# Kernel optimization log

Hardware: AMD Instinct MI355X
Metric: run time of the kernel (lower is better)

## Reference

```python
import jax, jax.numpy as jnp
import numpy as np

B, S, HIDDEN = 2, 2048, 2048
N_HEADS, N_KV_HEADS = 32, 8
HEAD_DIM = HIDDEN // N_HEADS          # 64
HALF = HEAD_DIM // 2                  # 32
N_REP = N_HEADS // N_KV_HEADS         # 4
NEG_INF = -1e9


def setup_inputs() -> dict:
    key = jax.random.key(0)
    ks = jax.random.split(key, 5)
    scale = 0.02
    x = jax.random.normal(ks[0], (B, S, HIDDEN), dtype=jnp.float32)
    wq = jax.random.normal(ks[1], (HIDDEN, N_HEADS * HEAD_DIM), dtype=jnp.float32) * scale
    wk = jax.random.normal(ks[2], (HIDDEN, N_KV_HEADS * HEAD_DIM), dtype=jnp.float32) * scale
    wv = jax.random.normal(ks[3], (HIDDEN, N_KV_HEADS * HEAD_DIM), dtype=jnp.float32) * scale
    wo = jax.random.normal(ks[4], (HIDDEN, HIDDEN), dtype=jnp.float32) * scale
    # Llama rotary frequencies: theta = 10000^{-2i/d}, angles = pos * theta
    inv_freq = 1.0 / (10000.0 ** (np.arange(0, HEAD_DIM, 2, dtype=np.float32) / HEAD_DIM))
    angles = np.arange(S, dtype=np.float32)[:, None] * inv_freq[None, :]  # [S, HALF]
    freqs_cos = jnp.asarray(np.cos(angles), dtype=jnp.float32)
    freqs_sin = jnp.asarray(np.sin(angles), dtype=jnp.float32)
    mask = jnp.tril(jnp.ones((S, S), dtype=bool))[None, None]  # causal [1,1,S,S]
    return {"x": x, "wq": wq, "wk": wk, "wv": wv, "wo": wo,
            "freqs_cos": freqs_cos, "freqs_sin": freqs_sin, "mask": mask}


def _apply_rope(t, cos, sin):
    # t: [B, S, H, HEAD_DIM]; cos/sin: [S, HALF] -> broadcast [1, S, 1, HALF]
    tr, ti = t[..., ::2], t[..., 1::2]           # real/imag halves (interleaved pairing)
    c = cos[None, :, None, :]
    s = sin[None, :, None, :]
    out_r = tr * c - ti * s
    out_i = tr * s + ti * c
    out = jnp.stack([out_r, out_i], axis=-1)     # [B,S,H,HALF,2]
    return out.reshape(t.shape)                  # re-interleave


def reference(x, wq, wk, wv, wo, freqs_cos, freqs_sin, mask):
    b, s, _ = x.shape
    xq = (x @ wq).reshape(b, s, N_HEADS, HEAD_DIM)
    xk = (x @ wk).reshape(b, s, N_KV_HEADS, HEAD_DIM)
    xv = (x @ wv).reshape(b, s, N_KV_HEADS, HEAD_DIM)
    xq = _apply_rope(xq, freqs_cos, freqs_sin)
    xk = _apply_rope(xk, freqs_cos, freqs_sin)
    # repeat_kv: interleave-repeat kv heads to match query heads
    xk = jnp.repeat(xk, N_REP, axis=2)           # [B,S,N_HEADS,HEAD_DIM]
    xv = jnp.repeat(xv, N_REP, axis=2)
    q = jnp.transpose(xq, (0, 2, 1, 3))          # [B,H,S,D]
    k = jnp.transpose(xk, (0, 2, 1, 3))
    v = jnp.transpose(xv, (0, 2, 1, 3))
    attn = jnp.einsum('bhqd,bhkd->bhqk', q, k) / jnp.sqrt(jnp.float32(HEAD_DIM))
    attn = attn + (1.0 - mask.astype(attn.dtype)) * NEG_INF  # keras Softmax masking
    attn = jax.nn.softmax(attn, axis=-1)
    out = jnp.einsum('bhqk,bhkd->bhqd', attn, v)
    out = jnp.transpose(out, (0, 2, 1, 3)).reshape(b, s, HIDDEN)
    return out @ wo
```

## Files before the change

kernel.cpp:

```cpp
#include <hip/hip_runtime.h>
#include <cstdint>
#include <cstddef>

#define S_LEN 2048
#define HIDDEN 2048
#define NH 32
#define NKV 8
#define HD 64
#define QKV_W 3072

typedef __bf16 bf16;
typedef __bf16 bf16x8 __attribute__((ext_vector_type(8)));
typedef __bf16 bf16x4 __attribute__((ext_vector_type(4)));
typedef float f32x4 __attribute__((ext_vector_type(4)));

__device__ __forceinline__ void async16(const bf16* g, bf16* l) {
  __builtin_amdgcn_global_load_lds((const __attribute__((address_space(1))) void*)g,
                                   (__attribute__((address_space(3))) void*)l, 16, 0, 0);
}

__device__ __forceinline__ int swz8(int row, int col) {
  return (((col >> 3) ^ (row & 7)) << 3) | (col & 7);
}

__global__ void cast_x_kernel(const float* __restrict__ in, bf16* __restrict__ out, int n4) {
  int i = blockIdx.x * blockDim.x + threadIdx.x;
  if (i >= n4) return;
  f32x4 v = ((const f32x4*)in)[i];
  bf16x4 o;
  o[0] = (bf16)v[0]; o[1] = (bf16)v[1]; o[2] = (bf16)v[2]; o[3] = (bf16)v[3];
  ((bf16x4*)out)[i] = o;
}

__global__ void transpose_cast_kernel(const float* __restrict__ in, bf16* __restrict__ out,
                                      int K, int N) {
  __shared__ float tile[32][33];
  const int n0 = blockIdx.x * 32, k0 = blockIdx.y * 32;
  const int tx = threadIdx.x, ty = threadIdx.y;
#pragma unroll
  for (int i = 0; i < 32; i += 8)
    tile[ty + i][tx] = in[(size_t)(k0 + ty + i) * N + n0 + tx];
  __syncthreads();
#pragma unroll
  for (int i = 0; i < 32; i += 8)
    out[(size_t)(n0 + ty + i) * K + k0 + tx] = (bf16)tile[tx][ty + i];
}

__global__ void vt_kernel(const bf16* __restrict__ qkv, bf16* __restrict__ vt) {
  __shared__ bf16 tile[32][33];
  const int s0 = blockIdx.x * 32, c0 = blockIdx.y * 32, b = blockIdx.z;
  const int tx = threadIdx.x, ty = threadIdx.y;
#pragma unroll
  for (int i = 0; i < 32; i += 8)
    tile[ty + i][tx] = qkv[((size_t)b * S_LEN + s0 + ty + i) * QKV_W + 2560 + c0 + tx];
  __syncthreads();
#pragma unroll
  for (int i = 0; i < 32; i += 8)
    vt[((size_t)b * 512 + c0 + ty + i) * S_LEN + s0 + tx] = tile[tx][ty + i];
}

template <int OUT_BF16>
__global__ __launch_bounds__(256) void gemm_bt_kernel(const bf16* __restrict__ A,
                                                      const bf16* __restrict__ Bt,
                                                      void* __restrict__ Cv,
                                                      int M, int N, int K) {
  __shared__ bf16 Al[128 * 32];
  __shared__ bf16 Bl[128 * 32];
  const int tid = threadIdx.x;
  const int lane = tid & 63, w = tid >> 6;
  const int quad = lane >> 4, l16 = lane & 15;
  const int m0 = blockIdx.y * 128, n0 = blockIdx.x * 128;
  const int wm = (w >> 1) * 64, wn = (w & 1) * 64;
  f32x4 acc[4][4] = {};
  const int srow = tid >> 2, scol = (tid & 3) * 8;
  const bf16* Ar0 = A + (size_t)(m0 + srow) * K + scol;
  const bf16* Ar1 = A + (size_t)(m0 + 64 + srow) * K + scol;
  const bf16* Br0 = Bt + (size_t)(n0 + srow) * K + scol;
  const bf16* Br1 = Bt + (size_t)(n0 + 64 + srow) * K + scol;
  bf16* al0 = Al + tid * 8;
  bf16* al1 = Al + 2048 + tid * 8;
  bf16* bl0 = Bl + tid * 8;
  bf16* bl1 = Bl + 2048 + tid * 8;
  for (int kt = 0; kt < K; kt += 32) {
    __syncthreads();
    async16(Ar0 + kt, al0);
    async16(Ar1 + kt, al1);
    async16(Br0 + kt, bl0);
    async16(Br1 + kt, bl1);
    __syncthreads();
    bf16x8 a[4], b[4];
#pragma unroll
    for (int mi = 0; mi < 4; ++mi)
      a[mi] = *(const bf16x8*)(Al + (wm + mi * 16 + l16) * 32 + quad * 8);
#pragma unroll
    for (int ni = 0; ni < 4; ++ni)
      b[ni] = *(const bf16x8*)(Bl + (wn + ni * 16 + l16) * 32 + quad * 8);
#pragma unroll
    for (int mi = 0; mi < 4; ++mi)
#pragma unroll
      for (int ni = 0; ni < 4; ++ni)
        acc[mi][ni] = __builtin_amdgcn_mfma_f32_16x16x32_bf16(a[mi], b[ni], acc[mi][ni], 0, 0, 0);
  }
#pragma unroll
  for (int mi = 0; mi < 4; ++mi)
#pragma unroll
    for (int ni = 0; ni < 4; ++ni)
#pragma unroll
      for (int i = 0; i < 4; ++i) {
        const int row = m0 + wm + mi * 16 + quad * 4 + i;
        const int col = n0 + wn + ni * 16 + l16;
        if (OUT_BF16)
          ((bf16*)Cv)[(size_t)row * N + col] = (bf16)acc[mi][ni][i];
        else
          ((float*)Cv)[(size_t)row * N + col] = acc[mi][ni][i];
      }
}

__global__ void rope_kernel(bf16* __restrict__ qkv, const float* __restrict__ cosp,
                            const float* __restrict__ sinp, int total) {
  int idx = blockIdx.x * blockDim.x + threadIdx.x;
  if (idx >= total) return;
  const int row = idx / 320;
  const int col = (idx - row * 320) * 8;
  const int s = row & (S_LEN - 1);
  const int j0 = (col >> 1) & 31;
  bf16* ptr = qkv + (size_t)row * QKV_W + col;
  bf16x8 v = *(bf16x8*)ptr;
#pragma unroll
  for (int u = 0; u < 4; ++u) {
    const float tr = (float)v[2 * u], ti = (float)v[2 * u + 1];
    const float c = cosp[s * 32 + j0 + u], sn = sinp[s * 32 + j0 + u];
    v[2 * u] = (bf16)(tr * c - ti * sn);
    v[2 * u + 1] = (bf16)(tr * sn + ti * c);
  }
  *(bf16x8*)ptr = v;
}

__global__ __launch_bounds__(256) void attn_kernel(const bf16* __restrict__ qkv,
                                                   const bf16* __restrict__ vt,
                                                   bf16* __restrict__ out) {
  __shared__ bf16 Kl[64 * 64];
  __shared__ bf16 Vl[64 * 64];
  __shared__ bf16 Pl[4][32 * 64];
  const int tid = threadIdx.x;
  const int lane = tid & 63, w = tid >> 6;
  const int quad = lane >> 4, l16 = lane & 15;
  int id = blockIdx.x;
  const int kvh = id & 7; id >>= 3;
  const int gx = id & 7; id >>= 3;
  const int rep = id & 3; const int b = id >> 2;
  const int h = kvh * 4 + rep;
  const bf16* Qbase = qkv + ((size_t)b * S_LEN) * QKV_W + h * HD;
  const bf16* Kbase = qkv + ((size_t)b * S_LEN) * QKV_W + 2048 + kvh * HD;
  const bf16* Vtb = vt + ((size_t)b * 512 + kvh * 64) * S_LEN;
  const int srow = tid >> 3;
  const int gcol = ((tid & 7) ^ (srow & 7)) * 8;
  const bf16* Ksrc0 = Kbase + (size_t)srow * QKV_W + gcol;
  const bf16* Ksrc1 = Kbase + (size_t)(srow + 32) * QKV_W + gcol;
  const bf16* Vsrc0 = Vtb + (size_t)srow * S_LEN + gcol;
  const bf16* Vsrc1 = Vtb + (size_t)(srow + 32) * S_LEN + gcol;

  for (int pass = 0; pass < 2; ++pass) {
    const int qt = pass ? (15 - gx) : gx;
    const int qbase = qt * 128 + w * 32;
    bf16x8 aq[2][2];
#pragma unroll
    for (int g = 0; g < 2; ++g) {
      const size_t qr = (size_t)(qbase + g * 16 + l16) * QKV_W;
      aq[g][0] = *(const bf16x8*)(Qbase + qr + quad * 8);
      aq[g][1] = *(const bf16x8*)(Qbase + qr + 32 + quad * 8);
    }
    float lsum0 = 0.f, lsum1 = 0.f;
    f32x4 o[2][4] = {};

    const int nt = 2 * qt + 2;
    for (int t = 0; t < nt; ++t) {
      const int kt = t * 64;
      __syncthreads();
      async16(Ksrc0 + (size_t)kt * QKV_W, Kl + tid * 8);
      async16(Ksrc1 + (size_t)kt * QKV_W, Kl + 2048 + tid * 8);
      async16(Vsrc0 + kt, Vl + tid * 8);
      async16(Vsrc1 + kt, Vl + 2048 + tid * 8);
      __syncthreads();
      const bool on0 = kt <= qbase + 15;
      const bool on1 = kt <= qbase + 31;
      if (!on1) continue;
      f32x4 c[2][4] = {};
#pragma unroll
      for (int j = 0; j < 4; ++j) {
        const int kr = j * 16 + l16;
        const bf16x8 bk0 = *(const bf16x8*)&Kl[kr * 64 + swz8(kr, quad * 8)];
        const bf16x8 bk1 = *(const bf16x8*)&Kl[kr * 64 + swz8(kr, 32 + quad * 8)];
        c[1][j] = __builtin_amdgcn_mfma_f32_16x16x32_bf16(bk0, aq[1][0], c[1][j], 0, 0, 0);
        c[1][j] = __builtin_amdgcn_mfma_f32_16x16x32_bf16(bk1, aq[1][1], c[1][j], 0, 0, 0);
        if (on0) {
          c[0][j] = __builtin_amdgcn_mfma_f32_16x16x32_bf16(bk0, aq[0][0], c[0][j], 0, 0, 0);
          c[0][j] = __builtin_amdgcn_mfma_f32_16x16x32_bf16(bk1, aq[0][1], c[0][j], 0, 0, 0);
        }
      }
#pragma unroll
      for (int g = 0; g < 2; ++g) {
        if (!(g ? on1 : on0)) continue;
        const int qrow = qbase + g * 16;
        float p[4][4];
#pragma unroll
        for (int j = 0; j < 4; ++j)
#pragma unroll
          for (int i = 0; i < 4; ++i)
            p[j][i] = exp2f(fmaf(c[g][j][i], 0.18033688f, -5.7707801f));
        if (kt + 63 > qrow) {
          const int qabs = qrow + l16;
#pragma unroll
          for (int j = 0; j < 4; ++j)
#pragma unroll
            for (int i = 0; i < 4; ++i)
              if (kt + j * 16 + quad * 4 + i > qabs) p[j][i] = 0.f;
        }
        float ls = 0.f;
#pragma unroll
        for (int j = 0; j < 4; ++j) {
          ls += (p[j][0] + p[j][1]) + (p[j][2] + p[j][3]);
          bf16x4 pv;
          pv[0] = (bf16)p[j][0]; pv[1] = (bf16)p[j][1];
          pv[2] = (bf16)p[j][2]; pv[3] = (bf16)p[j][3];
          const int pr = g * 16 + l16;
          *(bf16x4*)&Pl[w][pr * 64 + swz8(pr, j * 16 + quad * 4)] = pv;
        }
        if (g) lsum1 += ls; else lsum0 += ls;
      }
      bf16x8 ap0l, ap0h, ap1l, ap1h;
      {
        const int pr1 = 16 + l16;
        ap1l = *(const bf16x8*)&Pl[w][pr1 * 64 + swz8(pr1, quad * 8)];
        ap1h = *(const bf16x8*)&Pl[w][pr1 * 64 + swz8(pr1, 32 + quad * 8)];
        if (on0) {
          ap0l = *(const bf16x8*)&Pl[w][l16 * 64 + swz8(l16, quad * 8)];
          ap0h = *(const bf16x8*)&Pl[w][l16 * 64 + swz8(l16, 32 + quad * 8)];
        }
      }
#pragma unroll
      for (int dt = 0; dt < 4; ++dt) {
        const int vr = dt * 16 + l16;
        const bf16x8 bv0 = *(const bf16x8*)&Vl[vr * 64 + swz8(vr, quad * 8)];
        const bf16x8 bv1 = *(const bf16x8*)&Vl[vr * 64 + swz8(vr, 32 + quad * 8)];
        o[1][dt] = __builtin_amdgcn_mfma_f32_16x16x32_bf16(ap1l, bv0, o[1][dt], 0, 0, 0);
        o[1][dt] = __builtin_amdgcn_mfma_f32_16x16x32_bf16(ap1h, bv1, o[1][dt], 0, 0, 0);
        if (on0) {
          o[0][dt] = __builtin_amdgcn_mfma_f32_16x16x32_bf16(ap0l, bv0, o[0][dt], 0, 0, 0);
          o[0][dt] = __builtin_amdgcn_mfma_f32_16x16x32_bf16(ap0h, bv1, o[0][dt], 0, 0, 0);
        }
      }
    }
#pragma unroll
    for (int g = 0; g < 2; ++g) {
      float ls = g ? lsum1 : lsum0;
      ls += __shfl_xor(ls, 16);
      ls += __shfl_xor(ls, 32);
      const float rlq = 1.0f / ls;
#pragma unroll
      for (int i = 0; i < 4; ++i) {
        const float rl = __shfl(rlq, (lane & 48) | (quad * 4 + i));
        const int r = qbase + g * 16 + quad * 4 + i;
#pragma unroll
        for (int dt = 0; dt < 4; ++dt)
          out[((size_t)b * S_LEN + r) * HIDDEN + h * HD + dt * 16 + l16] =
              (bf16)(o[g][dt][i] * rl);
      }
    }
  }
}

extern "C" void kernel_launch(void* const* d_in, const int* in_sizes, int n_in,
                              void* d_out, int out_size, void* d_ws, size_t ws_size,
                              hipStream_t stream) {
  const float* x = (const float*)d_in[0];
  const float* wq = (const float*)d_in[1];
  const float* wk = (const float*)d_in[2];
  const float* wv = (const float*)d_in[3];
  const float* wo = (const float*)d_in[4];
  const float* fc = (const float*)d_in[5];
  const float* fs = (const float*)d_in[6];

  char* ws = (char*)d_ws;
  bf16* xb   = (bf16*)(ws);
  bf16* wT   = (bf16*)(ws + 16777216);
  bf16* woT  = (bf16*)(ws + 29360128);
  bf16* qkv  = (bf16*)(ws + 37748736);
  bf16* aout = (bf16*)(ws + 62914560);
  bf16* vt   = xb;

  cast_x_kernel<<<8192, 256, 0, stream>>>(x, xb, 2097152);
  transpose_cast_kernel<<<dim3(64, 64), dim3(32, 8), 0, stream>>>(wq, wT, 2048, 2048);
  transpose_cast_kernel<<<dim3(16, 64), dim3(32, 8), 0, stream>>>(wk, wT + (size_t)2048 * 2048, 2048, 512);
  transpose_cast_kernel<<<dim3(16, 64), dim3(32, 8), 0, stream>>>(wv, wT + (size_t)2560 * 2048, 2048, 512);
  transpose_cast_kernel<<<dim3(64, 64), dim3(32, 8), 0, stream>>>(wo, woT, 2048, 2048);

  gemm_bt_kernel<1><<<dim3(24, 32), 256, 0, stream>>>(xb, wT, (void*)qkv, 4096, 3072, 2048);
  rope_kernel<<<5120, 256, 0, stream>>>(qkv, fc, fs, 1310720);
  vt_kernel<<<dim3(64, 16, 2), dim3(32, 8), 0, stream>>>(qkv, vt);
  attn_kernel<<<512, 256, 0, stream>>>(qkv, vt, aout);
  gemm_bt_kernel<0><<<dim3(16, 32), 256, 0, stream>>>(aout, woT, d_out, 4096, 2048, 2048);
}
```

Measured before the change: 349.0 us.

## Double-buffer K/V tiles in attention kernel to overlap loads with compute

Moves the attention kernel from a single K/V shared-memory tile to two ping-pong buffers. The next tile's async global-to-LDS copy is issued before computing on the current tile, so there is one barrier per iteration instead of two. The aim is to hide global load latency behind the MFMA and softmax work. It doubles K/V LDS use, which may lower occupancy. It also relies on the end-of-iteration barrier being enough to make the async copy's data visible, which could be a correctness risk if the barrier does not wait for those copies to finish.

```diff
diff --git a/kernel.cpp b/kernel.cpp
--- a/kernel.cpp
+++ b/kernel.cpp
@@ -139,8 +139,8 @@
 __global__ __launch_bounds__(256) void attn_kernel(const bf16* __restrict__ qkv,
                                                    const bf16* __restrict__ vt,
                                                    bf16* __restrict__ out) {
-  __shared__ bf16 Kl[64 * 64];
-  __shared__ bf16 Vl[64 * 64];
+  __shared__ bf16 Kl[2][64 * 64];
+  __shared__ bf16 Vl[2][64 * 64];
   __shared__ bf16 Pl[4][32 * 64];
   const int tid = threadIdx.x;
   const int lane = tid & 63, w = tid >> 6;
@@ -174,82 +174,92 @@
     f32x4 o[2][4] = {};
 
     const int nt = 2 * qt + 2;
+    async16(Ksrc0, &Kl[0][tid * 8]);
+    async16(Ksrc1, &Kl[0][2048 + tid * 8]);
+    async16(Vsrc0, &Vl[0][tid * 8]);
+    async16(Vsrc1, &Vl[0][2048 + tid * 8]);
+    __syncthreads();
+
     for (int t = 0; t < nt; ++t) {
+      const int cur = t & 1;
+      if (t + 1 < nt) {
+        const int kn = (t + 1) * 64;
+        async16(Ksrc0 + (size_t)kn * QKV_W, &Kl[cur ^ 1][tid * 8]);
+        async16(Ksrc1 + (size_t)kn * QKV_W, &Kl[cur ^ 1][2048 + tid * 8]);
+        async16(Vsrc0 + kn, &Vl[cur ^ 1][tid * 8]);
+        async16(Vsrc1 + kn, &Vl[cur ^ 1][2048 + tid * 8]);
+      }
       const int kt = t * 64;
-      __syncthreads();
-      async16(Ksrc0 + (size_t)kt * QKV_W, Kl + tid * 8);
-      async16(Ksrc1 + (size_t)kt * QKV_W, Kl + 2048 + tid * 8);
-      async16(Vsrc0 + kt, Vl + tid * 8);
-      async16(Vsrc1 + kt, Vl + 2048 + tid * 8);
-      __syncthreads();
       const bool on0 = kt <= qbase + 15;
       const bool on1 = kt <= qbase + 31;
-      if (!on1) continue;
-      f32x4 c[2][4] = {};
-#pragma unroll
-      for (int j = 0; j < 4; ++j) {
-        const int kr = j * 16 + l16;
-        const bf16x8 bk0 = *(const bf16x8*)&Kl[kr * 64 + swz8(kr, quad * 8)];
-        const bf16x8 bk1 = *(const bf16x8*)&Kl[kr * 64 + swz8(kr, 32 + quad * 8)];
-        c[1][j] = __builtin_amdgcn_mfma_f32_16x16x32_bf16(bk0, aq[1][0], c[1][j], 0, 0, 0);
-        c[1][j] = __builtin_amdgcn_mfma_f32_16x16x32_bf16(bk1, aq[1][1], c[1][j], 0, 0, 0);
-        if (on0) {
-          c[0][j] = __builtin_amdgcn_mfma_f32_16x16x32_bf16(bk0, aq[0][0], c[0][j], 0, 0, 0);
-          c[0][j] = __builtin_amdgcn_mfma_f32_16x16x32_bf16(bk1, aq[0][1], c[0][j], 0, 0, 0);
+      if (on1) {
+        f32x4 c[2][4] = {};
+#pragma unroll
+        for (int j = 0; j < 4; ++j) {
+          const int kr = j * 16 + l16;
+          const bf16x8 bk0 = *(const bf16x8*)&Kl[cur][kr * 64 + swz8(kr, quad * 8)];
+          const bf16x8 bk1 = *(const bf16x8*)&Kl[cur][kr * 64 + swz8(kr, 32 + quad * 8)];
+          c[1][j] = __builtin_amdgcn_mfma_f32_16x16x32_bf16(bk0, aq[1][0], c[1][j], 0, 0, 0);
+          c[1][j] = __builtin_amdgcn_mfma_f32_16x16x32_bf16(bk1, aq[1][1], c[1][j], 0, 0, 0);
+          if (on0) {
+            c[0][j] = __builtin_amdgcn_mfma_f32_16x16x32_bf16(bk0, aq[0][0], c[0][j], 0, 0, 0);
+            c[0][j] = __builtin_amdgcn_mfma_f32_16x16x32_bf16(bk1, aq[0][1], c[0][j], 0, 0, 0);
+          }
+        }
+#pragma unroll
+        for (int g = 0; g < 2; ++g) {
+          if (!(g ? on1 : on0)) continue;
+          const int qrow = qbase + g * 16;
+          float p[4][4];
+#pragma unroll
+          for (int j = 0; j < 4; ++j)
+#pragma unroll
+            for (int i = 0; i < 4; ++i)
+              p[j][i] = exp2f(fmaf(c[g][j][i], 0.18033688f, -5.7707801f));
+          if (kt + 63 > qrow) {
+            const int qabs = qrow + l16;
+#pragma unroll
+            for (int j = 0; j < 4; ++j)
+#pragma unroll
+              for (int i = 0; i < 4; ++i)
+                if (kt + j * 16 + quad * 4 + i > qabs) p[j][i] = 0.f;
+          }
+          float ls = 0.f;
+#pragma unroll
+          for (int j = 0; j < 4; ++j) {
+            ls += (p[j][0] + p[j][1]) + (p[j][2] + p[j][3]);
+            bf16x4 pv;
+            pv[0] = (bf16)p[j][0]; pv[1] = (bf16)p[j][1];
+            pv[2] = (bf16)p[j][2]; pv[3] = (bf16)p[j][3];
+            const int pr = g * 16 + l16;
+            *(bf16x4*)&Pl[w][pr * 64 + swz8(pr, j * 16 + quad * 4)] = pv;
+          }
+          if (g) lsum1 += ls; else lsum0 += ls;
+        }
+        bf16x8 ap0l, ap0h, ap1l, ap1h;
+        {
+          const int pr1 = 16 + l16;
+          ap1l = *(const bf16x8*)&Pl[w][pr1 * 64 + swz8(pr1, quad * 8)];
+          ap1h = *(const bf16x8*)&Pl[w][pr1 * 64 + swz8(pr1, 32 + quad * 8)];
+          if (on0) {
+            ap0l = *(const bf16x8*)&Pl[w][l16 * 64 + swz8(l16, quad * 8)];
+            ap0h = *(const bf16x8*)&Pl[w][l16 * 64 + swz8(l16, 32 + quad * 8)];
+          }
+        }
+#pragma unroll
+        for (int dt = 0; dt < 4; ++dt) {
+          const int vr = dt * 16 + l16;
+          const bf16x8 bv0 = *(const bf16x8*)&Vl[cur][vr * 64 + swz8(vr, quad * 8)];
+          const bf16x8 bv1 = *(const bf16x8*)&Vl[cur][vr * 64 + swz8(vr, 32 + quad * 8)];
+          o[1][dt] = __builtin_amdgcn_mfma_f32_16x16x32_bf16(ap1l, bv0, o[1][dt], 0, 0, 0);
+          o[1][dt] = __builtin_amdgcn_mfma_f32_16x16x32_bf16(ap1h, bv1, o[1][dt], 0, 0, 0);
+          if (on0) {
+            o[0][dt] = __builtin_amdgcn_mfma_f32_16x16x32_bf16(ap0l, bv0, o[0][dt], 0, 0, 0);
+            o[0][dt] = __builtin_amdgcn_mfma_f32_16x16x32_bf16(ap0h, bv1, o[0][dt], 0, 0, 0);
+          }
         }
       }
-#pragma unroll
-      for (int g = 0; g < 2; ++g) {
-        if (!(g ? on1 : on0)) continue;
-        const int qrow = qbase + g * 16;
-        float p[4][4];
-#pragma unroll
-        for (int j = 0; j < 4; ++j)
-#pragma unroll
-          for (int i = 0; i < 4; ++i)
-            p[j][i] = exp2f(fmaf(c[g][j][i], 0.18033688f, -5.7707801f));
-        if (kt + 63 > qrow) {
-          const int qabs = qrow + l16;
-#pragma unroll
-          for (int j = 0; j < 4; ++j)
-#pragma unroll
-            for (int i = 0; i < 4; ++i)
-              if (kt + j * 16 + quad * 4 + i > qabs) p[j][i] = 0.f;
-        }
-        float ls = 0.f;
-#pragma unroll
-        for (int j = 0; j < 4; ++j) {
-          ls += (p[j][0] + p[j][1]) + (p[j][2] + p[j][3]);
-          bf16x4 pv;
-          pv[0] = (bf16)p[j][0]; pv[1] = (bf16)p[j][1];
-          pv[2] = (bf16)p[j][2]; pv[3] = (bf16)p[j][3];
-          const int pr = g * 16 + l16;
-          *(bf16x4*)&Pl[w][pr * 64 + swz8(pr, j * 16 + quad * 4)] = pv;
-        }
-        if (g) lsum1 += ls; else lsum0 += ls;
-      }
-      bf16x8 ap0l, ap0h, ap1l, ap1h;
-      {
-        const int pr1 = 16 + l16;
-        ap1l = *(const bf16x8*)&Pl[w][pr1 * 64 + swz8(pr1, quad * 8)];
-        ap1h = *(const bf16x8*)&Pl[w][pr1 * 64 + swz8(pr1, 32 + quad * 8)];
-        if (on0) {
-          ap0l = *(const bf16x8*)&Pl[w][l16 * 64 + swz8(l16, quad * 8)];
-          ap0h = *(const bf16x8*)&Pl[w][l16 * 64 + swz8(l16, 32 + quad * 8)];
-        }
-      }
-#pragma unroll
-      for (int dt = 0; dt < 4; ++dt) {
-        const int vr = dt * 16 + l16;
-        const bf16x8 bv0 = *(const bf16x8*)&Vl[vr * 64 + swz8(vr, quad * 8)];
-        const bf16x8 bv1 = *(const bf16x8*)&Vl[vr * 64 + swz8(vr, 32 + quad * 8)];
-        o[1][dt] = __builtin_amdgcn_mfma_f32_16x16x32_bf16(ap1l, bv0, o[1][dt], 0, 0, 0);
-        o[1][dt] = __builtin_amdgcn_mfma_f32_16x16x32_bf16(ap1h, bv1, o[1][dt], 0, 0, 0);
-        if (on0) {
-          o[0][dt] = __builtin_amdgcn_mfma_f32_16x16x32_bf16(ap0l, bv0, o[0][dt], 0, 0, 0);
-          o[0][dt] = __builtin_amdgcn_mfma_f32_16x16x32_bf16(ap0h, bv1, o[0][dt], 0, 0, 0);
-        }
-      }
+      __syncthreads();
     }
 #pragma unroll
     for (int g = 0; g < 2; ++g) {
```

New measurement: 349.8 us. No clear change (+0.2%).
